# Kernel tuning notes

Hardware: AMD Instinct MI355X
Metric: run time of the kernel (lower is better)

Reference implementation:

```python
import jax, jax.numpy as jnp
import numpy as np

HID, HEADS = 512, 8
C_DIM, H_DIM, W_DIM = 512, 64, 64
THETA = 100000000.0


def _angles(c, h, w, theta):
    # matches precompute_freqs_cis: angles whose polar form is freqs_cis
    n_f = c // 4
    freqs = 1.0 / theta ** (jnp.arange(0, c, 4)[:n_f].astype(jnp.float32) / c)  # (c//4,)
    th = jnp.arange(h, dtype=jnp.float32)
    tw = jnp.arange(w, dtype=jnp.float32)
    T = jnp.stack([jnp.broadcast_to(th[:, None], (h, w)),
                   jnp.broadcast_to(tw[None, :], (h, w))], axis=2)  # (h, w, 2)
    # torch cat [T*f0, T*f1, ...] along dim 2 == (h, w, c//4, 2) reshaped
    return (T[:, :, None, :] * freqs[None, None, :, None]).reshape(h, w, c // 2)


def setup_inputs() -> dict:
    key = jax.random.key(0)
    ks = jax.random.split(key, 9)
    B, S = 2, H_DIM * W_DIM
    s = 0.02
    return {
        "query": jax.random.normal(ks[0], (B, S, HID), jnp.float32),
        "key": jax.random.normal(ks[1], (B, S, HID), jnp.float32),
        "value": jax.random.normal(ks[2], (B, S, HID), jnp.float32),
        "Wq": jax.random.normal(ks[3], (HID, HID), jnp.float32) * s,
        "bq": jax.random.normal(ks[4], (HID,), jnp.float32) * s,
        "Wk": jax.random.normal(ks[5], (HID, HID), jnp.float32) * s,
        "bk": jax.random.normal(ks[6], (HID,), jnp.float32) * s,
        "Wv": jax.random.normal(ks[7], (HID, HID), jnp.float32) * s,
        "bv": jax.random.normal(ks[8], (HID,), jnp.float32) * s,
        "h": H_DIM,
        "w": W_DIM,
        "c": HID,
    }


def reference(query, key, value, Wq, bq, Wk, bk, Wv, bv, h, w, c):
    B = query.shape[0]
    hd = HID // HEADS
    ang = _angles(C_DIM, H_DIM, W_DIM, THETA)[:h, :w].reshape(h * w, c // 2)
    cos, sin = jnp.cos(ang), jnp.sin(ang)  # (S, c//2)

    Q = query @ Wq.T + bq
    K = key @ Wk.T + bk
    V = value @ Wv.T + bv

    def rot(x):  # complex multiply on consecutive pairs, in real arithmetic
        x2 = x.reshape(B, -1, c // 2, 2)
        xr, xi = x2[..., 0], x2[..., 1]
        return jnp.stack([xr * cos - xi * sin, xr * sin + xi * cos], axis=-1).reshape(B, -1, c)

    Q, K = rot(Q), rot(K)

    def heads(x):
        return x.reshape(B, -1, HEADS, hd).transpose(0, 2, 1, 3)  # (B, H, S, hd)

    Qh, Kh, Vh = heads(Q), heads(K), heads(V)
    # NOTE: original divides by head_dim (self.scale), not sqrt(head_dim)
    att = jnp.einsum('bhqd,bhkd->bhqk', Qh, Kh) / hd
    att = jax.nn.softmax(att, axis=-1)
    out = jnp.einsum('bhqk,bhkd->bhqd', att, Vh)
    return out.transpose(0, 2, 1, 3).reshape(B, -1, HID)
```

## Files before the change

### kernel.cpp

```cpp
#include <hip/hip_runtime.h>
#include <hip/hip_bf16.h>

#define S_LEN 4096
#define HDIM  64
#define NH    8

#define XFRAG_OFF 0
#define WFRAG_OFF 12582912
#define QKV_OFF   13369344
#define WS_NEED_BYTES ((size_t)(13369344 + 12582912) * 2)
#define FB_NEED_BYTES ((size_t)12582912 * 2)

typedef short s16x8 __attribute__((ext_vector_type(8)));
typedef float f32x16 __attribute__((ext_vector_type(16)));
typedef unsigned short u16x4 __attribute__((ext_vector_type(4)));

union FragU {
    s16x8 v;
    unsigned int u[4];
    unsigned short h[8];
};

static __device__ __forceinline__ unsigned int pack2_bf16(float a, float b) {
    __hip_bfloat162 h2 = __float22bfloat162_rn(float2{a, b});
    union { __hip_bfloat162 h; unsigned int u; } cv;
    cv.h = h2;
    return cv.u;
}

static __device__ __forceinline__ unsigned short to_bf16(float a) {
    __hip_bfloat16 h = __float2bfloat16(a);
    union { __hip_bfloat16 h; unsigned short u; } cv;
    cv.h = h;
    return cv.u;
}

#define Q_PRESCALE 0.022542110f
#define FREQ_L2 0.20762050593046f

__global__ __launch_bounds__(256) void conv_frag(
    const float* __restrict__ a, const float* __restrict__ b,
    const float* __restrict__ c, unsigned short* __restrict__ dst,
    int zstride)
{
    const int z = blockIdx.z;
    const float* src = (z == 0) ? a : ((z == 1) ? b : c);
    const size_t base = ((size_t)blockIdx.x * 256 + threadIdx.x) * 8;
    const int row = (int)(base >> 9);
    const int k   = (int)(base & 511);
    const int kc  = k >> 4;
    const int hi  = (k >> 3) & 1;

    const float4* p = (const float4*)(src + base);
    float4 x0 = p[0], x1 = p[1];
    FragU f;
    f.u[0] = pack2_bf16(x0.x, x0.y);
    f.u[1] = pack2_bf16(x0.z, x0.w);
    f.u[2] = pack2_bf16(x1.x, x1.y);
    f.u[3] = pack2_bf16(x1.z, x1.w);
    const size_t off = (size_t)z * zstride + (size_t)(row >> 5) * 16384
                     + kc * 512 + (hi * 32 + (row & 31)) * 8;
    *(s16x8*)(dst + off) = f.v;
}

static __device__ __forceinline__ void qkv_epilogue(
    int z, const f32x16 acc[2][2], int m0, int n0, int c31, int hi,
    const float* __restrict__ bias, unsigned short* __restrict__ dst_base)
{
    if (z < 2) {
        unsigned short* dst = dst_base + (size_t)z * 4194304;
        #pragma unroll
        for (int nt = 0; nt < 2; ++nt) {
            const int s_g = n0 + nt * 32 + c31;
            const int b   = s_g >> 12;
            const int s   = s_g & 4095;
            const float pos0 = (float)(s >> 6);
            const float pos1 = (float)(s & 63);
            #pragma unroll
            for (int mt = 0; mt < 2; ++mt) {
                #pragma unroll
                for (int g = 0; g < 4; ++g) {
                    const int o_b = m0 + mt * 32 + 8 * g + 4 * hi;
                    const float4 bb = *(const float4*)(bias + o_b);
                    float v0 = acc[mt][nt][4 * g + 0] + bb.x;
                    float v1 = acc[mt][nt][4 * g + 1] + bb.y;
                    float v2 = acc[mt][nt][4 * g + 2] + bb.z;
                    float v3 = acc[mt][nt][4 * g + 3] + bb.w;
                    const float fr0 = exp2f(-(float)(o_b >> 2) * FREQ_L2);
                    const float fr1 = exp2f(-(float)((o_b + 2) >> 2) * FREQ_L2);
                    float sn0, cs0, sn1, cs1;
                    __sincosf(pos0 * fr0, &sn0, &cs0);
                    __sincosf(pos1 * fr1, &sn1, &cs1);
                    float r0 = v0 * cs0 - v1 * sn0;
                    float r1 = v0 * sn0 + v1 * cs0;
                    float r2 = v2 * cs1 - v3 * sn1;
                    float r3 = v2 * sn1 + v3 * cs1;
                    if (z == 0) { r0 *= Q_PRESCALE; r1 *= Q_PRESCALE; r2 *= Q_PRESCALE; r3 *= Q_PRESCALE; }
                    const int bh = b * NH + (o_b >> 6);
                    const int k6 = o_b & 63;
                    u16x4 pk;
                    pk.x = to_bf16(r0); pk.y = to_bf16(r1);
                    pk.z = to_bf16(r2); pk.w = to_bf16(r3);
                    const size_t off = (size_t)bh * 262144 + (s >> 5) * 2048
                                     + (k6 >> 4) * 512 + (((k6 >> 3) & 1) * 32 + (s & 31)) * 8 + (k6 & 7);
                    *(u16x4*)(dst + off) = pk;
                }
            }
        }
    } else {
        unsigned short* dst = dst_base + 8388608;
        #pragma unroll
        for (int nt = 0; nt < 2; ++nt) {
            const int o  = n0 + nt * 32 + c31;
            const float bv_ = bias[o];
            const int d = o & 63, hh = o >> 6;
            #pragma unroll
            for (int mt = 0; mt < 2; ++mt) {
                #pragma unroll
                for (int g = 0; g < 4; ++g) {
                    const int s_b = m0 + mt * 32 + 8 * g + 4 * hi;
                    const int b = s_b >> 12;
                    const int s = s_b & 4095;
                    const int bh = b * NH + hh;
                    u16x4 pk;
                    pk.x = to_bf16(acc[mt][nt][4 * g + 0] + bv_);
                    pk.y = to_bf16(acc[mt][nt][4 * g + 1] + bv_);
                    pk.z = to_bf16(acc[mt][nt][4 * g + 2] + bv_);
                    pk.w = to_bf16(acc[mt][nt][4 * g + 3] + bv_);
                    const size_t off = (size_t)bh * 262144 + (s >> 5) * 2048 + (d >> 5) * 1024
                                     + ((s >> 4) & 1) * 512 + (((s >> 3) & 1) * 32 + (d & 31)) * 8 + (s & 7);
                    *(u16x4*)(dst + off) = pk;
                }
            }
        }
    }
}

__global__ __launch_bounds__(256) void qkv_gemm_rope(
    const unsigned short* __restrict__ xf, const unsigned short* __restrict__ wf,
    const float* __restrict__ bq, const float* __restrict__ bk,
    const float* __restrict__ bv, unsigned short* __restrict__ dst_base)
{
    const int z = blockIdx.z;
    const float* bias = (z == 0) ? bq : ((z == 1) ? bk : bv);
    const unsigned short* X = xf + (size_t)z * 4194304;
    const unsigned short* W = wf + (size_t)z * 262144;

    const int tid  = threadIdx.x;
    const int wv   = tid >> 6;
    const int lane = tid & 63;
    const int c31  = lane & 31;
    const int hi   = lane >> 5;
    const int wm   = wv >> 1, wn = wv & 1;

    int m0, n0;
    const unsigned short *A, *B;
    if (z < 2) {
        m0 = blockIdx.y * 128 + wm * 64;
        n0 = blockIdx.x * 128 + wn * 64;
        A = W; B = X;
    } else {
        m0 = blockIdx.x * 128 + wm * 64;
        n0 = blockIdx.y * 128 + wn * 64;
        A = X; B = W;
    }

    const unsigned short* ap0 = A + (size_t)(m0 >> 5) * 16384 + lane * 8;
    const unsigned short* ap1 = ap0 + 16384;
    const unsigned short* bp0 = B + (size_t)(n0 >> 5) * 16384 + lane * 8;
    const unsigned short* bp1 = bp0 + 16384;

    f32x16 acc[2][2];
    #pragma unroll
    for (int a = 0; a < 2; ++a)
    #pragma unroll
    for (int b = 0; b < 2; ++b)
    #pragma unroll
    for (int r = 0; r < 16; ++r) acc[a][b][r] = 0.f;

    #pragma unroll 4
    for (int kc = 0; kc < 32; ++kc) {
        const int ko = kc * 512;
        s16x8 a0 = *(const s16x8*)(ap0 + ko);
        s16x8 a1 = *(const s16x8*)(ap1 + ko);
        s16x8 b0 = *(const s16x8*)(bp0 + ko);
        s16x8 b1 = *(const s16x8*)(bp1 + ko);
        acc[0][0] = __builtin_amdgcn_mfma_f32_32x32x16_bf16(a0, b0, acc[0][0], 0, 0, 0);
        acc[0][1] = __builtin_amdgcn_mfma_f32_32x32x16_bf16(a0, b1, acc[0][1], 0, 0, 0);
        acc[1][0] = __builtin_amdgcn_mfma_f32_32x32x16_bf16(a1, b0, acc[1][0], 0, 0, 0);
        acc[1][1] = __builtin_amdgcn_mfma_f32_32x32x16_bf16(a1, b1, acc[1][1], 0, 0, 0);
    }

    qkv_epilogue(z, acc, m0, n0, c31, hi, bias, dst_base);
}

__global__ __launch_bounds__(256) void qkv_rope_f32(
    const float* __restrict__ q_in, const float* __restrict__ k_in,
    const float* __restrict__ v_in,
    const float* __restrict__ Wq, const float* __restrict__ bq,
    const float* __restrict__ Wk, const float* __restrict__ bk,
    const float* __restrict__ Wv, const float* __restrict__ bv,
    unsigned short* __restrict__ dst_base)
{
    const int z = blockIdx.z;
    const float* Xr = (z == 0) ? q_in : ((z == 1) ? k_in : v_in);
    const float* Wr = (z == 0) ? Wq   : ((z == 1) ? Wk   : Wv);
    const float* bias = (z == 0) ? bq : ((z == 1) ? bk : bv);

    const int tid  = threadIdx.x;
    const int wv   = tid >> 6;
    const int lane = tid & 63;
    const int c31  = lane & 31;
    const int hi   = lane >> 5;
    const int wm   = wv >> 1, wn = wv & 1;

    int m0, n0;
    const float *A, *B;
    if (z < 2) { m0 = blockIdx.y * 128 + wm * 64; n0 = blockIdx.x * 128 + wn * 64; A = Wr; B = Xr; }
    else       { m0 = blockIdx.x * 128 + wm * 64; n0 = blockIdx.y * 128 + wn * 64; A = Xr; B = Wr; }

    f32x16 acc[2][2];
    #pragma unroll
    for (int a = 0; a < 2; ++a)
    #pragma unroll
    for (int b = 0; b < 2; ++b)
    #pragma unroll
    for (int r = 0; r < 16; ++r) acc[a][b][r] = 0.f;

    for (int kc = 0; kc < 32; ++kc) {
        const int kofs = kc * 16 + hi * 8;
        FragU a_f[2], b_f[2];
        #pragma unroll
        for (int mt = 0; mt < 2; ++mt) {
            const float4* p = (const float4*)(A + (size_t)(m0 + mt * 32 + c31) * 512 + kofs);
            float4 x0 = p[0], x1 = p[1];
            a_f[mt].u[0] = pack2_bf16(x0.x, x0.y);
            a_f[mt].u[1] = pack2_bf16(x0.z, x0.w);
            a_f[mt].u[2] = pack2_bf16(x1.x, x1.y);
            a_f[mt].u[3] = pack2_bf16(x1.z, x1.w);
        }
        #pragma unroll
        for (int nt = 0; nt < 2; ++nt) {
            const float4* p = (const float4*)(B + (size_t)(n0 + nt * 32 + c31) * 512 + kofs);
            float4 x0 = p[0], x1 = p[1];
            b_f[nt].u[0] = pack2_bf16(x0.x, x0.y);
            b_f[nt].u[1] = pack2_bf16(x0.z, x0.w);
            b_f[nt].u[2] = pack2_bf16(x1.x, x1.y);
            b_f[nt].u[3] = pack2_bf16(x1.z, x1.w);
        }
        #pragma unroll
        for (int mt = 0; mt < 2; ++mt)
        #pragma unroll
        for (int nt = 0; nt < 2; ++nt)
            acc[mt][nt] = __builtin_amdgcn_mfma_f32_32x32x16_bf16(
                a_f[mt].v, b_f[nt].v, acc[mt][nt], 0, 0, 0);
    }

    qkv_epilogue(z, acc, m0, n0, c31, hi, bias, dst_base);
}

__global__ __launch_bounds__(256, 3) void flash_attn_st(
    const unsigned short* __restrict__ qkv, float* __restrict__ out)
{
    __shared__ __align__(16) unsigned char smem[33792];
    float* sOb = (float*)smem;
    float* sL  = (float*)(smem + 32768);

    const int tid  = threadIdx.x;
    const int wv   = tid >> 6;
    const int lane = tid & 63;
    const int c31  = lane & 31;
    const int hi   = lane >> 5;
    const int q0   = blockIdx.x * 64;
    const int bh   = blockIdx.y;

    const unsigned short* Qb  = qkv + (size_t)bh * 262144;
    const unsigned short* Kb  = qkv + (size_t)4194304 + (size_t)bh * 262144;
    const unsigned short* Vtb = qkv + (size_t)8388608 + (size_t)bh * 262144;

    s16x8 qf[2][4];
    #pragma unroll
    for (int qt = 0; qt < 2; ++qt)
    #pragma unroll
    for (int kc = 0; kc < 4; ++kc)
        qf[qt][kc] = *(const s16x8*)(Qb + (size_t)((q0 >> 5) + qt) * 2048 + kc * 512 + lane * 8);

    f32x16 o_acc[2][2];
    #pragma unroll
    for (int a = 0; a < 2; ++a)
    #pragma unroll
    for (int b = 0; b < 2; ++b)
    #pragma unroll
    for (int r = 0; r < 16; ++r) o_acc[a][b][r] = 0.f;
    float l_acc[2] = {0.f, 0.f};

    const unsigned short* kp = Kb  + (size_t)wv * 2048 + lane * 8;
    const unsigned short* vp = Vtb + (size_t)wv * 2048 + lane * 8;

    s16x8 ka[4];
    #pragma unroll
    for (int kc = 0; kc < 4; ++kc)
        ka[kc] = *(const s16x8*)(kp + kc * 512);

    for (int it = 0; it < 32; ++it) {
        s16x8 va[2][2];
        va[0][0] = *(const s16x8*)(vp);
        va[0][1] = *(const s16x8*)(vp + 512);
        va[1][0] = *(const s16x8*)(vp + 1024);
        va[1][1] = *(const s16x8*)(vp + 1536);
        vp += 8192;

        unsigned int up[2][8];

        {
            f32x16 st;
            #pragma unroll
            for (int r = 0; r < 16; ++r) st[r] = 0.f;
            #pragma unroll
            for (int kc = 0; kc < 4; ++kc)
                st = __builtin_amdgcn_mfma_f32_32x32x16_bf16(ka[kc], qf[0][kc], st, 0, 0, 0);
            float ls0 = 0.f, ls1 = 0.f;
            #pragma unroll
            for (int qq = 0; qq < 8; ++qq) {
                float p0 = __builtin_amdgcn_exp2f(st[2 * qq]);
                float p1 = __builtin_amdgcn_exp2f(st[2 * qq + 1]);
                ls0 += p0; ls1 += p1;
                up[0][qq] = pack2_bf16(p0, p1);
            }
            l_acc[0] += ls0 + ls1;
        }

        f32x16 st;
        #pragma unroll
        for (int r = 0; r < 16; ++r) st[r] = 0.f;
        #pragma unroll
        for (int kc = 0; kc < 4; ++kc)
            st = __builtin_amdgcn_mfma_f32_32x32x16_bf16(ka[kc], qf[1][kc], st, 0, 0, 0);

        kp += 8192;
        if (it < 31) {
            #pragma unroll
            for (int kc = 0; kc < 4; ++kc)
                ka[kc] = *(const s16x8*)(kp + kc * 512);
        }

        {
            float ls0 = 0.f, ls1 = 0.f;
            #pragma unroll
            for (int qq = 0; qq < 8; ++qq) {
                float p0 = __builtin_amdgcn_exp2f(st[2 * qq]);
                float p1 = __builtin_amdgcn_exp2f(st[2 * qq + 1]);
                ls0 += p0; ls1 += p1;
                up[1][qq] = pack2_bf16(p0, p1);
            }
            l_acc[1] += ls0 + ls1;
        }

        #pragma unroll
        for (int qt = 0; qt < 2; ++qt) {
            #pragma unroll
            for (int k2 = 0; k2 < 2; ++k2) {
                const unsigned int a0 = up[qt][4 * k2 + 0];
                const unsigned int a1 = up[qt][4 * k2 + 1];
                const unsigned int a2 = up[qt][4 * k2 + 2];
                const unsigned int a3 = up[qt][4 * k2 + 3];
                const unsigned int s0 = (unsigned int)__shfl_xor((int)(hi ? a0 : a2), 32);
                const unsigned int s1 = (unsigned int)__shfl_xor((int)(hi ? a1 : a3), 32);
                FragU pb;
                pb.u[0] = hi ? s0 : a0;
                pb.u[1] = hi ? s1 : a1;
                pb.u[2] = hi ? a2 : s0;
                pb.u[3] = hi ? a3 : s1;
                #pragma unroll
                for (int dt = 0; dt < 2; ++dt)
                    o_acc[dt][qt] = __builtin_amdgcn_mfma_f32_32x32x16_bf16(
                        va[dt][k2], pb.v, o_acc[dt][qt], 0, 0, 0);
            }
        }
    }

    {
        float l0 = l_acc[0] + __shfl_xor(l_acc[0], 32);
        float l1 = l_acc[1] + __shfl_xor(l_acc[1], 32);
        if (lane < 32) {
            sL[(wv * 2 + 0) * 32 + lane] = l0;
            sL[(wv * 2 + 1) * 32 + lane] = l1;
        }
    }
    __syncthreads();

    if (wv == 1 || wv == 2) {
        float* buf = sOb + (wv - 1) * 4096;
        #pragma unroll
        for (int dt = 0; dt < 2; ++dt)
        #pragma unroll
        for (int qt = 0; qt < 2; ++qt)
        #pragma unroll
        for (int r = 0; r < 16; ++r) {
            const int d = dt * 32 + (r & 3) + 8 * (r >> 2) + 4 * hi;
            buf[d * 64 + qt * 32 + c31] = o_acc[dt][qt][r];
        }
    }
    __syncthreads();
    if (wv == 0 || wv == 3) {
        const float* buf = sOb + ((wv == 0) ? 0 : 4096);
        #pragma unroll
        for (int dt = 0; dt < 2; ++dt)
        #pragma unroll
        for (int qt = 0; qt < 2; ++qt)
        #pragma unroll
        for (int r = 0; r < 16; ++r) {
            const int d = dt * 32 + (r & 3) + 8 * (r >> 2) + 4 * hi;
            o_acc[dt][qt][r] += buf[d * 64 + qt * 32 + c31];
        }
    }
    __syncthreads();
    if (wv == 3) {
        #pragma unroll
        for (int dt = 0; dt < 2; ++dt)
        #pragma unroll
        for (int qt = 0; qt < 2; ++qt)
        #pragma unroll
        for (int r = 0; r < 16; ++r) {
            const int d = dt * 32 + (r & 3) + 8 * (r >> 2) + 4 * hi;
            sOb[d * 64 + qt * 32 + c31] = o_acc[dt][qt][r];
        }
    }
    __syncthreads();
    if (wv == 0) {
        #pragma unroll
        for (int dt = 0; dt < 2; ++dt)
        #pragma unroll
        for (int qt = 0; qt < 2; ++qt)
        #pragma unroll
        for (int r = 0; r < 16; ++r) {
            const int d = dt * 32 + (r & 3) + 8 * (r >> 2) + 4 * hi;
            o_acc[dt][qt][r] += sOb[d * 64 + qt * 32 + c31];
        }
        const int b  = bh >> 3;
        const int hh = bh & 7;
        #pragma unroll
        for (int qt = 0; qt < 2; ++qt) {
            const float lsum = sL[(0 * 2 + qt) * 32 + c31] + sL[(1 * 2 + qt) * 32 + c31]
                             + sL[(2 * 2 + qt) * 32 + c31] + sL[(3 * 2 + qt) * 32 + c31];
            const float rinv = 1.f / lsum;
            const int s = q0 + qt * 32 + c31;
            float* orow = out + ((size_t)b * S_LEN + s) * 512 + hh * 64;
            #pragma unroll
            for (int dt = 0; dt < 2; ++dt) {
                #pragma unroll
                for (int g = 0; g < 4; ++g) {
                    float4 vv;
                    vv.x = o_acc[dt][qt][4 * g + 0] * rinv;
                    vv.y = o_acc[dt][qt][4 * g + 1] * rinv;
                    vv.z = o_acc[dt][qt][4 * g + 2] * rinv;
                    vv.w = o_acc[dt][qt][4 * g + 3] * rinv;
                    *(float4*)(orow + dt * 32 + 8 * g + 4 * hi) = vv;
                }
            }
        }
    }
}

extern "C" void kernel_launch(void* const* d_in, const int* in_sizes, int n_in,
                              void* d_out, int out_size, void* d_ws, size_t ws_size,
                              hipStream_t stream) {
    (void)in_sizes; (void)n_in; (void)out_size;
    const float* q_in = (const float*)d_in[0];
    const float* k_in = (const float*)d_in[1];
    const float* v_in = (const float*)d_in[2];
    const float* Wq   = (const float*)d_in[3];
    const float* bq   = (const float*)d_in[4];
    const float* Wk   = (const float*)d_in[5];
    const float* bk   = (const float*)d_in[6];
    const float* Wv   = (const float*)d_in[7];
    const float* bv   = (const float*)d_in[8];
    unsigned short* ws = (unsigned short*)d_ws;
    float* out = (float*)d_out;

    if (ws_size >= WS_NEED_BYTES) {
        conv_frag<<<dim3(2048, 1, 3), 256, 0, stream>>>(q_in, k_in, v_in, ws + XFRAG_OFF, 4194304);
        conv_frag<<<dim3(128, 1, 3), 256, 0, stream>>>(Wq, Wk, Wv, ws + WFRAG_OFF, 262144);
        qkv_gemm_rope<<<dim3(64, 4, 3), 256, 0, stream>>>(
            ws + XFRAG_OFF, ws + WFRAG_OFF, bq, bk, bv, ws + QKV_OFF);
        flash_attn_st<<<dim3(64, 16), 256, 0, stream>>>(ws + QKV_OFF, out);
    } else {
        qkv_rope_f32<<<dim3(64, 4, 3), 256, 0, stream>>>(
            q_in, k_in, v_in, Wq, bq, Wk, bk, Wv, bv, ws);
        flash_attn_st<<<dim3(64, 16), 256, 0, stream>>>(ws, out);
    }
}
```

Measured before the change: 236.9 us.

## Split attention waves across query and key halves, merge conversion kernels

The attention kernel now assigns each wave one 32-row query tile and half of the key blocks, instead of each wave covering both query tiles over a quarter of the keys. Q is staged in shared memory, and the cross-wave reduction shrinks to one pairwise merge. Occupancy is raised to 4 blocks per SM, trading more loop iterations per wave for fewer live registers and less reduction work. Separately, the two bf16 fragment-conversion launches are merged into one kernel, and a redundant exp2 in the RoPE epilogue is dropped because both pairs share the same frequency.

New measurement: 236.1 us. About the same (-0.3%).

```diff
diff --git a/kernel.cpp b/kernel.cpp
--- a/kernel.cpp
+++ b/kernel.cpp
@@ -38,29 +38,44 @@
 #define Q_PRESCALE 0.022542110f
 #define FREQ_L2 0.20762050593046f
 
-__global__ __launch_bounds__(256) void conv_frag(
-    const float* __restrict__ a, const float* __restrict__ b,
-    const float* __restrict__ c, unsigned short* __restrict__ dst,
-    int zstride)
+__global__ __launch_bounds__(256) void conv_frag2(
+    const float* __restrict__ qx, const float* __restrict__ kx,
+    const float* __restrict__ vx,
+    const float* __restrict__ Wq, const float* __restrict__ Wk,
+    const float* __restrict__ Wv,
+    unsigned short* __restrict__ xdst, unsigned short* __restrict__ wdst)
 {
-    const int z = blockIdx.z;
-    const float* src = (z == 0) ? a : ((z == 1) ? b : c);
-    const size_t base = ((size_t)blockIdx.x * 256 + threadIdx.x) * 8;
-    const int row = (int)(base >> 9);
-    const int k   = (int)(base & 511);
-    const int kc  = k >> 4;
-    const int hi  = (k >> 3) & 1;
-
-    const float4* p = (const float4*)(src + base);
-    float4 x0 = p[0], x1 = p[1];
-    FragU f;
-    f.u[0] = pack2_bf16(x0.x, x0.y);
-    f.u[1] = pack2_bf16(x0.z, x0.w);
-    f.u[2] = pack2_bf16(x1.x, x1.y);
-    f.u[3] = pack2_bf16(x1.z, x1.w);
-    const size_t off = (size_t)z * zstride + (size_t)(row >> 5) * 16384
-                     + kc * 512 + (hi * 32 + (row & 31)) * 8;
-    *(s16x8*)(dst + off) = f.v;
+    const int z  = blockIdx.z;
+    const int bx = blockIdx.x;
+    const int tid  = threadIdx.x;
+    const int wv   = tid >> 6;
+    const int lane = tid & 63;
+    const int row  = lane & 31;
+    const int hi   = lane >> 5;
+
+    const float* src;
+    unsigned short* dst;
+    if (bx < 256) {
+        src = ((z == 0) ? qx : ((z == 1) ? kx : vx)) + (size_t)(bx * 32 + row) * 512 + hi * 8;
+        dst = xdst + (size_t)z * 4194304 + (size_t)bx * 16384;
+    } else {
+        const int s = bx - 256;
+        src = ((z == 0) ? Wq : ((z == 1) ? Wk : Wv)) + (size_t)(s * 32 + row) * 512 + hi * 8;
+        dst = wdst + (size_t)z * 262144 + (size_t)s * 16384;
+    }
+
+    #pragma unroll
+    for (int i = 0; i < 8; ++i) {
+        const int kc = wv * 8 + i;
+        const float4* p = (const float4*)(src + kc * 16);
+        float4 x0 = p[0], x1 = p[1];
+        FragU f;
+        f.u[0] = pack2_bf16(x0.x, x0.y);
+        f.u[1] = pack2_bf16(x0.z, x0.w);
+        f.u[2] = pack2_bf16(x1.x, x1.y);
+        f.u[3] = pack2_bf16(x1.z, x1.w);
+        *(s16x8*)(dst + kc * 512 + lane * 8) = f.v;
+    }
 }
 
 static __device__ __forceinline__ void qkv_epilogue(
@@ -87,10 +102,9 @@
                     float v2 = acc[mt][nt][4 * g + 2] + bb.z;
                     float v3 = acc[mt][nt][4 * g + 3] + bb.w;
                     const float fr0 = exp2f(-(float)(o_b >> 2) * FREQ_L2);
-                    const float fr1 = exp2f(-(float)((o_b + 2) >> 2) * FREQ_L2);
                     float sn0, cs0, sn1, cs1;
                     __sincosf(pos0 * fr0, &sn0, &cs0);
-                    __sincosf(pos1 * fr1, &sn1, &cs1);
+                    __sincosf(pos1 * fr0, &sn1, &cs1);
                     float r0 = v0 * cs0 - v1 * sn0;
                     float r1 = v0 * sn0 + v1 * cs0;
                     float r2 = v2 * cs1 - v3 * sn1;
@@ -259,18 +273,21 @@
     qkv_epilogue(z, acc, m0, n0, c31, hi, bias, dst_base);
 }
 
-__global__ __launch_bounds__(256, 3) void flash_attn_st(
+__global__ __launch_bounds__(256, 4) void flash_attn_st(
     const unsigned short* __restrict__ qkv, float* __restrict__ out)
 {
-    __shared__ __align__(16) unsigned char smem[33792];
-    float* sOb = (float*)smem;
-    float* sL  = (float*)(smem + 32768);
+    __shared__ __align__(16) unsigned char smem[8192 + 16384 + 256];
+    unsigned short* sQ = (unsigned short*)smem;
+    float* sOb = (float*)(smem + 8192);
+    float* sL  = (float*)(smem + 8192 + 16384);
 
     const int tid  = threadIdx.x;
     const int wv   = tid >> 6;
     const int lane = tid & 63;
     const int c31  = lane & 31;
     const int hi   = lane >> 5;
+    const int qs   = wv >> 1;
+    const int ks   = wv & 1;
     const int q0   = blockIdx.x * 64;
     const int bh   = blockIdx.y;
 
@@ -278,185 +295,125 @@
     const unsigned short* Kb  = qkv + (size_t)4194304 + (size_t)bh * 262144;
     const unsigned short* Vtb = qkv + (size_t)8388608 + (size_t)bh * 262144;
 
-    s16x8 qf[2][4];
-    #pragma unroll
-    for (int qt = 0; qt < 2; ++qt)
-    #pragma unroll
-    for (int kc = 0; kc < 4; ++kc)
-        qf[qt][kc] = *(const s16x8*)(Qb + (size_t)((q0 >> 5) + qt) * 2048 + kc * 512 + lane * 8);
-
-    f32x16 o_acc[2][2];
-    #pragma unroll
-    for (int a = 0; a < 2; ++a)
-    #pragma unroll
-    for (int b = 0; b < 2; ++b)
-    #pragma unroll
-    for (int r = 0; r < 16; ++r) o_acc[a][b][r] = 0.f;
-    float l_acc[2] = {0.f, 0.f};
-
-    const unsigned short* kp = Kb  + (size_t)wv * 2048 + lane * 8;
-    const unsigned short* vp = Vtb + (size_t)wv * 2048 + lane * 8;
+    #pragma unroll
+    for (int i = 0; i < 2; ++i) {
+        const int idx   = tid + i * 256;
+        const int chunk = idx >> 6;
+        const int ln    = idx & 63;
+        *(s16x8*)(sQ + chunk * 512 + ln * 8) =
+            *(const s16x8*)(Qb + (size_t)((q0 >> 5) + (chunk >> 2)) * 2048 + (chunk & 3) * 512 + ln * 8);
+    }
+    __syncthreads();
+
+    const unsigned short* sQw = sQ + qs * 2048 + lane * 8;
+
+    f32x16 o_acc[2];
+    #pragma unroll
+    for (int dt = 0; dt < 2; ++dt)
+    #pragma unroll
+    for (int r = 0; r < 16; ++r) o_acc[dt][r] = 0.f;
+    float l_acc = 0.f;
+
+    const unsigned short* kp = Kb  + (size_t)ks * 2048 + lane * 8;
+    const unsigned short* vp = Vtb + (size_t)ks * 2048 + lane * 8;
 
     s16x8 ka[4];
     #pragma unroll
     for (int kc = 0; kc < 4; ++kc)
         ka[kc] = *(const s16x8*)(kp + kc * 512);
 
-    for (int it = 0; it < 32; ++it) {
+    for (int it = 0; it < 64; ++it) {
         s16x8 va[2][2];
         va[0][0] = *(const s16x8*)(vp);
         va[0][1] = *(const s16x8*)(vp + 512);
         va[1][0] = *(const s16x8*)(vp + 1024);
         va[1][1] = *(const s16x8*)(vp + 1536);
-        vp += 8192;
-
-        unsigned int up[2][8];
-
+        vp += 4096;
+
+        f32x16 st;
+        #pragma unroll
+        for (int r = 0; r < 16; ++r) st[r] = 0.f;
+        #pragma unroll
+        for (int kc = 0; kc < 4; ++kc) {
+            s16x8 qf = *(const s16x8*)(sQw + kc * 512);
+            st = __builtin_amdgcn_mfma_f32_32x32x16_bf16(ka[kc], qf, st, 0, 0, 0);
+        }
+
+        kp += 4096;
+        if (it < 63) {
+            #pragma unroll
+            for (int kc = 0; kc < 4; ++kc)
+                ka[kc] = *(const s16x8*)(kp + kc * 512);
+        }
+
+        unsigned int up[8];
         {
-            f32x16 st;
-            #pragma unroll
-            for (int r = 0; r < 16; ++r) st[r] = 0.f;
-            #pragma unroll
-            for (int kc = 0; kc < 4; ++kc)
-                st = __builtin_amdgcn_mfma_f32_32x32x16_bf16(ka[kc], qf[0][kc], st, 0, 0, 0);
             float ls0 = 0.f, ls1 = 0.f;
             #pragma unroll
             for (int qq = 0; qq < 8; ++qq) {
                 float p0 = __builtin_amdgcn_exp2f(st[2 * qq]);
                 float p1 = __builtin_amdgcn_exp2f(st[2 * qq + 1]);
                 ls0 += p0; ls1 += p1;
-                up[0][qq] = pack2_bf16(p0, p1);
+                up[qq] = pack2_bf16(p0, p1);
             }
-            l_acc[0] += ls0 + ls1;
-        }
-
-        f32x16 st;
-        #pragma unroll
-        for (int r = 0; r < 16; ++r) st[r] = 0.f;
-        #pragma unroll
-        for (int kc = 0; kc < 4; ++kc)
-            st = __builtin_amdgcn_mfma_f32_32x32x16_bf16(ka[kc], qf[1][kc], st, 0, 0, 0);
-
-        kp += 8192;
-        if (it < 31) {
-            #pragma unroll
-            for (int kc = 0; kc < 4; ++kc)
-                ka[kc] = *(const s16x8*)(kp + kc * 512);
-        }
-
-        {
-            float ls0 = 0.f, ls1 = 0.f;
-            #pragma unroll
-            for (int qq = 0; qq < 8; ++qq) {
-                float p0 = __builtin_amdgcn_exp2f(st[2 * qq]);
-                float p1 = __builtin_amdgcn_exp2f(st[2 * qq + 1]);
-                ls0 += p0; ls1 += p1;
-                up[1][qq] = pack2_bf16(p0, p1);
-            }
-            l_acc[1] += ls0 + ls1;
-        }
-
-        #pragma unroll
-        for (int qt = 0; qt < 2; ++qt) {
-            #pragma unroll
-            for (int k2 = 0; k2 < 2; ++k2) {
-                const unsigned int a0 = up[qt][4 * k2 + 0];
-                const unsigned int a1 = up[qt][4 * k2 + 1];
-                const unsigned int a2 = up[qt][4 * k2 + 2];
-                const unsigned int a3 = up[qt][4 * k2 + 3];
-                const unsigned int s0 = (unsigned int)__shfl_xor((int)(hi ? a0 : a2), 32);
-                const unsigned int s1 = (unsigned int)__shfl_xor((int)(hi ? a1 : a3), 32);
-                FragU pb;
-                pb.u[0] = hi ? s0 : a0;
-                pb.u[1] = hi ? s1 : a1;
-                pb.u[2] = hi ? a2 : s0;
-                pb.u[3] = hi ? a3 : s1;
-                #pragma unroll
-                for (int dt = 0; dt < 2; ++dt)
-                    o_acc[dt][qt] = __builtin_amdgcn_mfma_f32_32x32x16_bf16(
-                        va[dt][k2], pb.v, o_acc[dt][qt], 0, 0, 0);
-            }
-        }
-    }
-
-    {
-        float l0 = l_acc[0] + __shfl_xor(l_acc[0], 32);
-        float l1 = l_acc[1] + __shfl_xor(l_acc[1], 32);
-        if (lane < 32) {
-            sL[(wv * 2 + 0) * 32 + lane] = l0;
-            sL[(wv * 2 + 1) * 32 + lane] = l1;
-        }
-    }
-    __syncthreads();
-
-    if (wv == 1 || wv == 2) {
-        float* buf = sOb + (wv - 1) * 4096;
+            l_acc += ls0 + ls1;
+        }
+
+        #pragma unroll
+        for (int k2 = 0; k2 < 2; ++k2) {
+            const unsigned int a0 = up[4 * k2 + 0];
+            const unsigned int a1 = up[4 * k2 + 1];
+            const unsigned int a2 = up[4 * k2 + 2];
+            const unsigned int a3 = up[4 * k2 + 3];
+            const unsigned int s0 = (unsigned int)__shfl_xor((int)(hi ? a0 : a2), 32);
+            const unsigned int s1 = (unsigned int)__shfl_xor((int)(hi ? a1 : a3), 32);
+            FragU pb;
+            pb.u[0] = hi ? s0 : a0;
+            pb.u[1] = hi ? s1 : a1;
+            pb.u[2] = hi ? a2 : s0;
+            pb.u[3] = hi ? a3 : s1;
+            #pragma unroll
+            for (int dt = 0; dt < 2; ++dt)
+                o_acc[dt] = __builtin_amdgcn_mfma_f32_32x32x16_bf16(
+                    va[dt][k2], pb.v, o_acc[dt], 0, 0, 0);
+        }
+    }
+
+    const float lw = l_acc + __shfl_xor(l_acc, 32);
+    if (ks == 1) {
+        if (lane < 32) sL[qs * 32 + lane] = lw;
         #pragma unroll
         for (int dt = 0; dt < 2; ++dt)
-        #pragma unroll
-        for (int qt = 0; qt < 2; ++qt)
         #pragma unroll
         for (int r = 0; r < 16; ++r) {
             const int d = dt * 32 + (r & 3) + 8 * (r >> 2) + 4 * hi;
-            buf[d * 64 + qt * 32 + c31] = o_acc[dt][qt][r];
+            sOb[qs * 2048 + d * 32 + c31] = o_acc[dt][r];
         }
     }
     __syncthreads();
-    if (wv == 0 || wv == 3) {
-        const float* buf = sOb + ((wv == 0) ? 0 : 4096);
+    if (ks == 0) {
         #pragma unroll
         for (int dt = 0; dt < 2; ++dt)
-        #pragma unroll
-        for (int qt = 0; qt < 2; ++qt)
         #pragma unroll
         for (int r = 0; r < 16; ++r) {
             const int d = dt * 32 + (r & 3) + 8 * (r >> 2) + 4 * hi;
-            o_acc[dt][qt][r] += buf[d * 64 + qt * 32 + c31];
-        }
-    }
-    __syncthreads();
-    if (wv == 3) {
-        #pragma unroll
-        for (int dt = 0; dt < 2; ++dt)
-        #pragma unroll
-        for (int qt = 0; qt < 2; ++qt)
-        #pragma unroll
-        for (int r = 0; r < 16; ++r) {
-            const int d = dt * 32 + (r & 3) + 8 * (r >> 2) + 4 * hi;
-            sOb[d * 64 + qt * 32 + c31] = o_acc[dt][qt][r];
-        }
-    }
-    __syncthreads();
-    if (wv == 0) {
-        #pragma unroll
-        for (int dt = 0; dt < 2; ++dt)
-        #pragma unroll
-        for (int qt = 0; qt < 2; ++qt)
-        #pragma unroll
-        for (int r = 0; r < 16; ++r) {
-            const int d = dt * 32 + (r & 3) + 8 * (r >> 2) + 4 * hi;
-            o_acc[dt][qt][r] += sOb[d * 64 + qt * 32 + c31];
-        }
+            o_acc[dt][r] += sOb[qs * 2048 + d * 32 + c31];
+        }
+        const float rinv = 1.f / (lw + sL[qs * 32 + c31]);
         const int b  = bh >> 3;
         const int hh = bh & 7;
-        #pragma unroll
-        for (int qt = 0; qt < 2; ++qt) {
-            const float lsum = sL[(0 * 2 + qt) * 32 + c31] + sL[(1 * 2 + qt) * 32 + c31]
-                             + sL[(2 * 2 + qt) * 32 + c31] + sL[(3 * 2 + qt) * 32 + c31];
-            const float rinv = 1.f / lsum;
-            const int s = q0 + qt * 32 + c31;
-            float* orow = out + ((size_t)b * S_LEN + s) * 512 + hh * 64;
-            #pragma unroll
-            for (int dt = 0; dt < 2; ++dt) {
-                #pragma unroll
-                for (int g = 0; g < 4; ++g) {
-                    float4 vv;
-                    vv.x = o_acc[dt][qt][4 * g + 0] * rinv;
-                    vv.y = o_acc[dt][qt][4 * g + 1] * rinv;
-                    vv.z = o_acc[dt][qt][4 * g + 2] * rinv;
-                    vv.w = o_acc[dt][qt][4 * g + 3] * rinv;
-                    *(float4*)(orow + dt * 32 + 8 * g + 4 * hi) = vv;
-                }
+        const int s  = q0 + qs * 32 + c31;
+        float* orow = out + ((size_t)b * S_LEN + s) * 512 + hh * 64;
+        #pragma unroll
+        for (int dt = 0; dt < 2; ++dt) {
+            #pragma unroll
+            for (int g = 0; g < 4; ++g) {
+                float4 vv;
+                vv.x = o_acc[dt][4 * g + 0] * rinv;
+                vv.y = o_acc[dt][4 * g + 1] * rinv;
+                vv.z = o_acc[dt][4 * g + 2] * rinv;
+                vv.w = o_acc[dt][4 * g + 3] * rinv;
+                *(float4*)(orow + dt * 32 + 8 * g + 4 * hi) = vv;
             }
         }
     }
@@ -479,8 +436,8 @@
     float* out = (float*)d_out;
 
     if (ws_size >= WS_NEED_BYTES) {
-        conv_frag<<<dim3(2048, 1, 3), 256, 0, stream>>>(q_in, k_in, v_in, ws + XFRAG_OFF, 4194304);
-        conv_frag<<<dim3(128, 1, 3), 256, 0, stream>>>(Wq, Wk, Wv, ws + WFRAG_OFF, 262144);
+        conv_frag2<<<dim3(272, 1, 3), 256, 0, stream>>>(
+            q_in, k_in, v_in, Wq, Wk, Wv, ws + XFRAG_OFF, ws + WFRAG_OFF);
         qkv_gemm_rope<<<dim3(64, 4, 3), 256, 0, stream>>>(
             ws + XFRAG_OFF, ws + WFRAG_OFF, bq, bk, bv, ws + QKV_OFF);
         flash_attn_st<<<dim3(64, 16), 256, 0, stream>>>(ws + QKV_OFF, out);
```
